# Performance work log

Measured on AMD Instinct MI355X. Metric: run time of the kernel, lower is better.

Reference implementation:

```python
import jax, jax.numpy as jnp
import numpy as np
from jax import lax

EPS_LN = 1e-5
EPS_NORM = 1e-12
NUM_HEADS = 8
KV_HEADS = 2
REP = NUM_HEADS // KV_HEADS


def _layernorm_c(x, w, b):
    # WithBias LayerNorm over channel dim; x: [b,c,h,w]
    mu = x.mean(axis=1, keepdims=True)
    var = ((x - mu) ** 2).mean(axis=1, keepdims=True)
    return (x - mu) / jnp.sqrt(var + EPS_LN) * w[None, :, None, None] + b[None, :, None, None]


def _conv1x1(x, w):
    # x: [b,c,h,w], w: [o,c]
    return jnp.einsum('bchw,oc->bohw', x, w)


def _dwconv3x3(x, w):
    # depthwise 3x3, SAME padding; w: [C,1,3,3]
    C = x.shape[1]
    return lax.conv_general_dilated(
        x, w, window_strides=(1, 1), padding='SAME',
        dimension_numbers=('NCHW', 'OIHW', 'NCHW'), feature_group_count=C)


def _l2norm(x):
    # normalize over last axis (torch F.normalize semantics)
    n = jnp.sqrt(jnp.sum(x * x, axis=-1, keepdims=True))
    return x / jnp.maximum(n, EPS_NORM)


def setup_inputs() -> dict:
    key = jax.random.key(0)
    ks = jax.random.split(key, 8)
    b, dim, h, w = 4, 192, 256, 256
    kv_ch = 2 * dim // REP  # 96
    return {
        'x': jax.random.normal(ks[0], (b, dim, h, w), jnp.float32),
        'ln_w': jnp.ones((dim,), jnp.float32),
        'ln_b': jnp.zeros((dim,), jnp.float32),
        'q_w': jax.random.normal(ks[1], (dim, dim), jnp.float32) * 0.02,
        'q_dw': jax.random.normal(ks[2], (dim, 1, 3, 3), jnp.float32) * 0.1,
        'kv_w': jax.random.normal(ks[3], (kv_ch, dim), jnp.float32) * 0.02,
        'kv_dw': jax.random.normal(ks[4], (kv_ch, 1, 3, 3), jnp.float32) * 0.1,
        'proj_w': jax.random.normal(ks[5], (dim, dim), jnp.float32) * 0.02,
        'temperature': jnp.ones((NUM_HEADS, 1, 1), jnp.float32),
    }


def reference(x, ln_w, ln_b, q_w, q_dw, kv_w, kv_dw, proj_w, temperature):
    b, c, h, w = x.shape
    xn = _layernorm_c(x, ln_w, ln_b)
    q = _dwconv3x3(_conv1x1(xn, q_w), q_dw)            # [b, c, h, w]
    kv = _dwconv3x3(_conv1x1(xn, kv_w), kv_dw)         # [b, 2c/rep, h, w]
    k, v = jnp.split(kv, 2, axis=1)
    hw = h * w
    ch = c // NUM_HEADS
    q = q.reshape(b, NUM_HEADS, ch, hw)
    k = k.reshape(b, KV_HEADS, ch, hw)
    v = v.reshape(b, KV_HEADS, ch, hw)
    k = jnp.repeat(k, REP, axis=1)                     # repeat_kv
    v = jnp.repeat(v, REP, axis=1)
    q = _l2norm(q)
    k = _l2norm(k)
    attn = jnp.einsum('bhcn,bhdn->bhcd', q, k) * temperature[None]
    attn = jax.nn.softmax(attn, axis=-1)
    out = jnp.einsum('bhcd,bhdn->bhcn', attn, v)
    out = out.reshape(b, c, h, w)
    return _conv1x1(out, proj_w)
```

## Files before the change

### kernel.cpp

```cpp
#include <hip/hip_runtime.h>
#include <hip/hip_bf16.h>
#include <stdint.h>

#define HW    65536
#define NB    4
#define CIN   192
#define OYC   288
#define BSTR  200
#define EPS2  264

__device__ __forceinline__ float bflo(unsigned u){ return __uint_as_float(u << 16); }
__device__ __forceinline__ float bfhi(unsigned u){ return __uint_as_float(u & 0xffff0000u); }
__device__ __forceinline__ float bf2f(__hip_bfloat16 v){ return __bfloat162float(v); }
__device__ __forceinline__ unsigned short f2bfbits(float f){
  __hip_bfloat16 h = __float2bfloat16(f); return *(unsigned short*)&h;
}

__device__ __forceinline__ void unpack8(uint4 u, float* f) {
  f[0]=bflo(u.x); f[1]=bfhi(u.x); f[2]=bflo(u.y); f[3]=bfhi(u.y);
  f[4]=bflo(u.z); f[5]=bfhi(u.z); f[6]=bflo(u.w); f[7]=bfhi(u.w);
}

union BF8 { uint4 u; __hip_bfloat16 h[8]; };

typedef __attribute__((ext_vector_type(8))) short short8;
typedef __attribute__((ext_vector_type(4))) float floatx4;

__global__ void k_prep(const float* __restrict__ qw, const float* __restrict__ kvw,
                       const float* __restrict__ lnw, const float* __restrict__ lnb,
                       __hip_bfloat16* __restrict__ AF, float* __restrict__ bias,
                       float* __restrict__ Ssum) {
  int blk = blockIdx.x, t = threadIdx.x;
  if (blk < 32) {
    for (int i = blk * 256 + t; i < OYC * CIN; i += 32 * 256) {
      int o = i / CIN, c = i % CIN;
      float w = (o < 192) ? qw[o * 192 + c] : kvw[(o - 192) * 192 + c];
      float val = w * lnw[c];
      int ot = o >> 4, lo = o & 15;
      int ks = c >> 5, cr = c & 31, q = cr >> 3, j = cr & 7;
      int dst = (((ot * 6 + ks) * 64) + q * 16 + lo) * 8 + j;
      AF[dst] = __float2bfloat16(val);
    }
  } else {
    for (int o = t; o < OYC; o += 256) {
      float s = 0.f, s2 = 0.f;
      for (int c = 0; c < CIN; ++c) {
        float w = (o < 192) ? qw[o * 192 + c] : kvw[(o - 192) * 192 + c];
        s += w * lnb[c];
        s2 += bf2f(__float2bfloat16(w * lnw[c]));
      }
      bias[o] = s;
      Ssum[o] = s2;
    }
  }
}

__global__ __launch_bounds__(512, 2) void k_conv1r(const float* __restrict__ x,
                                                   const __hip_bfloat16* __restrict__ AF,
                                                   const float* __restrict__ bias,
                                                   const float* __restrict__ Ssum,
                                                   __hip_bfloat16* __restrict__ y) {
  __shared__ __align__(16) __hip_bfloat16 Bl[256 * BSTR];
  __shared__ float part_s[8][256];
  __shared__ float part_q[8][256];
  __shared__ float murs[256][2];
  __shared__ float biasl[OYC];
  __shared__ float Sl[OYC];

  int bid = blockIdx.x;
  int b = bid >> 8;
  int r = bid & 255;
  int tid = threadIdx.x;
  int w = tid >> 6, l = tid & 63;

  for (int i = tid; i < OYC; i += 512) { biasl[i] = bias[i]; Sl[i] = Ssum[i]; }

  {
    const float* xb = x + (size_t)(b * CIN + w * 24) * HW + r * 256 + l * 4;
    float s[4] = {0.f, 0.f, 0.f, 0.f}, q2[4] = {0.f, 0.f, 0.f, 0.f};
    unsigned pk[4][12];
#pragma unroll
    for (int c = 0; c < 24; ++c) {
      float4 v4 = *(const float4*)(xb + (size_t)c * HW);
      float vv[4] = {v4.x, v4.y, v4.z, v4.w};
#pragma unroll
      for (int i = 0; i < 4; ++i) {
        s[i] += vv[i]; q2[i] += vv[i] * vv[i];
        unsigned bits = f2bfbits(vv[i]);
        if ((c & 1) == 0) pk[i][c >> 1] = bits;
        else              pk[i][c >> 1] |= bits << 16;
      }
    }
#pragma unroll
    for (int i = 0; i < 4; ++i) {
      int px = l * 4 + i;
#pragma unroll
      for (int j = 0; j < 3; ++j) {
        uint4 u = make_uint4(pk[i][j*4], pk[i][j*4+1], pk[i][j*4+2], pk[i][j*4+3]);
        *(uint4*)&Bl[px * BSTR + w * 24 + j * 8] = u;
      }
    }
    *(float4*)&part_s[w][l * 4] = make_float4(s[0], s[1], s[2], s[3]);
    *(float4*)&part_q[w][l * 4] = make_float4(q2[0], q2[1], q2[2], q2[3]);
  }
  __syncthreads();

  int lane = tid & 63;
  int mh = w >> 2, nq = w & 3;
  int li = lane & 15, qd = lane >> 4;

  floatx4 acc[9][4];
#pragma unroll
  for (int t = 0; t < 9; ++t)
#pragma unroll
    for (int nt = 0; nt < 4; ++nt) acc[t][nt] = (floatx4){0.f, 0.f, 0.f, 0.f};

  const __hip_bfloat16* abase = AF + ((size_t)(mh * 9) * 6 * 64 + lane) * 8;
  short8 a0[9], a1[9];
#pragma unroll
  for (int t = 0; t < 9; ++t) a0[t] = *(const short8*)(abase + (size_t)(t * 6) * 512);

#pragma unroll
  for (int ks = 0; ks < 6; ++ks) {
    short8 bf[4];
#pragma unroll
    for (int nt = 0; nt < 4; ++nt) {
      int px = nq * 64 + nt * 16 + li;
      bf[nt] = *(const short8*)&Bl[px * BSTR + ks * 32 + qd * 8];
    }
    if (ks < 5) {
#pragma unroll
      for (int t = 0; t < 9; ++t) {
        short8 v = *(const short8*)(abase + (size_t)(t * 6 + ks + 1) * 512);
        if (ks & 1) a0[t] = v; else a1[t] = v;
      }
    }
#pragma unroll
    for (int t = 0; t < 9; ++t) {
      short8 af = (ks & 1) ? a1[t] : a0[t];
#pragma unroll
      for (int nt = 0; nt < 4; ++nt)
        acc[t][nt] = __builtin_amdgcn_mfma_f32_16x16x32_bf16(af, bf[nt], acc[t][nt], 0, 0, 0);
    }
  }

  if (tid < 256) {
    float s0 = 0.f, s1 = 0.f;
#pragma unroll
    for (int g = 0; g < 8; ++g) { s0 += part_s[g][tid]; s1 += part_q[g][tid]; }
    float m = s0 * (1.f / CIN);
    float var = s1 * (1.f / CIN) - m * m;
    murs[tid][0] = m;
    murs[tid][1] = rsqrtf(var + 1e-5f);
  }

  __hip_bfloat16* EP = Bl;
#pragma unroll
  for (int ph = 0; ph < 2; ++ph) {
    __syncthreads();
    if (mh == ph) {
#pragma unroll
      for (int t = 0; t < 9; ++t)
#pragma unroll
        for (int nt = 0; nt < 4; ++nt) {
          int px = nq * 64 + nt * 16 + li;
          float mu = murs[px][0], rs = murs[px][1];
#pragma unroll
          for (int rr = 0; rr < 4; ++rr) {
            int ol = t * 16 + qd * 4 + rr;
            float val = rs * (acc[t][nt][rr] - mu * Sl[ph * 144 + ol]) + biasl[ph * 144 + ol];
            EP[ol * EPS2 + px] = __float2bfloat16(val);
          }
        }
    }
    __syncthreads();
    for (int i = tid; i < 144 * 32; i += 512) {
      int row = i >> 5, seg = i & 31;
      uint4 u = *(const uint4*)&EP[row * EPS2 + seg * 8];
      *(uint4*)&y[(size_t)(b * OYC + ph * 144 + row) * HW + r * 256 + seg * 8] = u;
    }
  }
}

__global__ __launch_bounds__(256) void k_dwkv(const __hip_bfloat16* __restrict__ y,
                                              const float* __restrict__ kvdw,
                                              __hip_bfloat16* __restrict__ kbuf,
                                              __hip_bfloat16* __restrict__ vbuf,
                                              float* __restrict__ kss) {
  __shared__ __align__(16) __hip_bfloat16 stage[18 * 256];
  int bid = blockIdx.x;
  int hb = bid & 15;
  int ck = (bid >> 4) % 96;
  int b  = bid / (16 * 96);
  int tid = threadIdx.x;
  int h0 = hb * 16;

  const __hip_bfloat16* yp = y + (size_t)(b * OYC + 192 + ck) * HW;
  for (int i = tid; i < 18 * 32; i += 256) {
    int ry = i >> 5, seg = i & 31;
    int hh = h0 - 1 + ry;
    uint4 u = make_uint4(0u, 0u, 0u, 0u);
    if ((unsigned)hh < 256u) u = *(const uint4*)(yp + hh * 256 + seg * 8);
    *(uint4*)&stage[ry * 256 + seg * 8] = u;
  }
  __syncthreads();

  float w[9];
#pragma unroll
  for (int i = 0; i < 9; ++i) w[i] = kvdw[ck * 9 + i];

  int cg = tid & 31, rg = tid >> 5;
  int c0 = cg * 8;
  bool isk = (ck < 48);
  __hip_bfloat16* ob = (isk ? kbuf : vbuf) + (size_t)(b * 48 + (ck % 48)) * HW;
  float ssq = 0.f;
#pragma unroll
  for (int rr = 0; rr < 2; ++rr) {
    int orow = rg * 2 + rr;
    float o[8];
#pragma unroll
    for (int j = 0; j < 8; ++j) o[j] = 0.f;
#pragma unroll
    for (int ry = 0; ry < 3; ++ry) {
      const __hip_bfloat16* rb = &stage[(orow + ry) * 256];
      float v[8];
      unpack8(*(const uint4*)&rb[c0], v);
      float vl = (c0 > 0)       ? bf2f(rb[c0 - 1]) : 0.f;
      float vr = (c0 + 8 < 256) ? bf2f(rb[c0 + 8]) : 0.f;
      float wl = w[ry * 3], wm = w[ry * 3 + 1], wr = w[ry * 3 + 2];
      o[0] = fmaf(wl, vl, fmaf(wm, v[0], fmaf(wr, v[1], o[0])));
#pragma unroll
      for (int j = 1; j < 7; ++j)
        o[j] = fmaf(wl, v[j-1], fmaf(wm, v[j], fmaf(wr, v[j+1], o[j])));
      o[7] = fmaf(wl, v[6], fmaf(wm, v[7], fmaf(wr, vr, o[7])));
    }
    BF8 t;
#pragma unroll
    for (int j = 0; j < 8; ++j) {
      t.h[j] = __float2bfloat16(o[j]);
      if (isk) { float fv = bf2f(t.h[j]); ssq += fv * fv; }
    }
    *(uint4*)(ob + (size_t)(h0 + orow) * 256 + c0) = t.u;
  }
  if (isk) {
#pragma unroll
    for (int off = 32; off > 0; off >>= 1) ssq += __shfl_down(ssq, off);
    __shared__ float ws4[4];
    if ((tid & 63) == 0) ws4[tid >> 6] = ssq;
    __syncthreads();
    if (tid == 0) atomicAdd(&kss[b * 48 + ck], ws4[0] + ws4[1] + ws4[2] + ws4[3]);
  }
}

__global__ __launch_bounds__(256) void k_dwq(const __hip_bfloat16* __restrict__ y,
                                             const float* __restrict__ qdw,
                                             __hip_bfloat16* __restrict__ qfull,
                                             float* __restrict__ qss) {
  __shared__ __align__(16) __hip_bfloat16 stage[18 * 256];
  int bid = blockIdx.x;
  int hb = bid & 15;
  int c  = (bid >> 4) % 192;
  int b  = bid / (16 * 192);
  int tid = threadIdx.x;
  int h0 = hb * 16;

  const __hip_bfloat16* yp = y + (size_t)(b * OYC + c) * HW;
  for (int i = tid; i < 18 * 32; i += 256) {
    int ry = i >> 5, seg = i & 31;
    int hh = h0 - 1 + ry;
    uint4 u = make_uint4(0u, 0u, 0u, 0u);
    if ((unsigned)hh < 256u) u = *(const uint4*)(yp + hh * 256 + seg * 8);
    *(uint4*)&stage[ry * 256 + seg * 8] = u;
  }
  __syncthreads();

  float w[9];
#pragma unroll
  for (int i = 0; i < 9; ++i) w[i] = qdw[c * 9 + i];

  int cg = tid & 31, rg = tid >> 5;
  int c0 = cg * 8;
  __hip_bfloat16* ob = qfull + (size_t)(b * CIN + c) * HW;
  float ssq = 0.f;
#pragma unroll
  for (int rr = 0; rr < 2; ++rr) {
    int orow = rg * 2 + rr;
    float o[8];
#pragma unroll
    for (int j = 0; j < 8; ++j) o[j] = 0.f;
#pragma unroll
    for (int ry = 0; ry < 3; ++ry) {
      const __hip_bfloat16* rb = &stage[(orow + ry) * 256];
      float v[8];
      unpack8(*(const uint4*)&rb[c0], v);
      float vl = (c0 > 0)       ? bf2f(rb[c0 - 1]) : 0.f;
      float vr = (c0 + 8 < 256) ? bf2f(rb[c0 + 8]) : 0.f;
      float wl = w[ry * 3], wm = w[ry * 3 + 1], wr = w[ry * 3 + 2];
      o[0] = fmaf(wl, vl, fmaf(wm, v[0], fmaf(wr, v[1], o[0])));
#pragma unroll
      for (int j = 1; j < 7; ++j)
        o[j] = fmaf(wl, v[j-1], fmaf(wm, v[j], fmaf(wr, v[j+1], o[j])));
      o[7] = fmaf(wl, v[6], fmaf(wm, v[7], fmaf(wr, vr, o[7])));
    }
    BF8 t;
#pragma unroll
    for (int j = 0; j < 8; ++j) {
      t.h[j] = __float2bfloat16(o[j]);
      float fv = bf2f(t.h[j]); ssq += fv * fv;
    }
    *(uint4*)(ob + (size_t)(h0 + orow) * 256 + c0) = t.u;
  }
#pragma unroll
  for (int off = 32; off > 0; off >>= 1) ssq += __shfl_down(ssq, off);
  __shared__ float ws4[4];
  if ((tid & 63) == 0) ws4[tid >> 6] = ssq;
  __syncthreads();
  if (tid == 0) atomicAdd(&qss[b * 192 + c], ws4[0] + ws4[1] + ws4[2] + ws4[3]);
}

__global__ __launch_bounds__(256) void k_qk(const __hip_bfloat16* __restrict__ qfull,
                                            const __hip_bfloat16* __restrict__ kbuf,
                                            float* __restrict__ attn) {
  __shared__ float red[96 * 33];
  int bid = blockIdx.x;
  int ck  = bid & 63;
  int kvh = (bid >> 6) & 1;
  int b   = bid >> 7;
  int tid = threadIdx.x;
  int wave = tid >> 6, lane = tid & 63;
  int li = lane & 15, qd = lane >> 4;

  for (int i = tid; i < 96 * 33; i += 256) red[i] = 0.f;

  const __hip_bfloat16* qp = qfull + (size_t)(b * CIN + kvh * 96) * HW;
  const __hip_bfloat16* kp = kbuf  + (size_t)(b * 48 + kvh * 24) * HW;
  int n0 = ck * 1024 + wave * 256;

  floatx4 acc[6][2];
#pragma unroll
  for (int mt = 0; mt < 6; ++mt) {
    acc[mt][0] = (floatx4){0.f, 0.f, 0.f, 0.f};
    acc[mt][1] = (floatx4){0.f, 0.f, 0.f, 0.f};
  }

  int kr1 = 16 + li; if (kr1 > 23) kr1 = 23;
  for (int ks = 0; ks < 8; ++ks) {
    int nn = n0 + ks * 32 + qd * 8;
    short8 bk0 = *(const short8*)(kp + (size_t)li  * HW + nn);
    short8 bk1 = *(const short8*)(kp + (size_t)kr1 * HW + nn);
#pragma unroll
    for (int mt = 0; mt < 6; ++mt) {
      short8 aq = *(const short8*)(qp + (size_t)(mt * 16 + li) * HW + nn);
      acc[mt][0] = __builtin_amdgcn_mfma_f32_16x16x32_bf16(aq, bk0, acc[mt][0], 0, 0, 0);
      acc[mt][1] = __builtin_amdgcn_mfma_f32_16x16x32_bf16(aq, bk1, acc[mt][1], 0, 0, 0);
    }
  }
  __syncthreads();

#pragma unroll
  for (int mt = 0; mt < 6; ++mt) {
#pragma unroll
    for (int nt = 0; nt < 2; ++nt) {
      int n = nt * 16 + li;
      if (n < 24) {
#pragma unroll
        for (int r = 0; r < 4; ++r) {
          int m = mt * 16 + qd * 4 + r;
          atomicAdd(&red[m * 33 + n], acc[mt][nt][r]);
        }
      }
    }
  }
  __syncthreads();

  for (int i = tid; i < 96 * 24; i += 256) {
    int m = i / 24, d = i % 24;
    int head = kvh * 4 + m / 24, cp = m % 24;
    atomicAdd(&attn[(((b * 8 + head) * 24) + cp) * 24 + d], red[m * 33 + d]);
  }
}

__global__ void k_attn_final(const float* __restrict__ attn, const float* __restrict__ qss,
                             const float* __restrict__ kss, const float* __restrict__ temp,
                             const float* __restrict__ projw, float* __restrict__ Mt) {
  int b = blockIdx.x;
  int t = threadIdx.x;
  __shared__ float as_[96 * 25];
  float acc[48];
#pragma unroll
  for (int j = 0; j < 48; ++j) acc[j] = 0.f;
  for (int kvh = 0; kvh < 2; ++kvh) {
    __syncthreads();
    if (t < 96) {
      int row = kvh * 96 + t;
      int h = row / 24, cp = row % 24;
      float rq = 1.f / fmaxf(sqrtf(qss[b * 192 + row]), 1e-12f);
      float tp = temp[h];
      float lg[24]; float mx = -1e30f;
#pragma unroll
      for (int d = 0; d < 24; ++d) {
        float rk = 1.f / fmaxf(sqrtf(kss[b * 48 + kvh * 24 + d]), 1e-12f);
        float l = attn[(((b * 8 + h) * 24) + cp) * 24 + d] * rq * rk * tp;
        lg[d] = l; mx = fmaxf(mx, l);
      }
      float s = 0.f;
#pragma unroll
      for (int d = 0; d < 24; ++d) { lg[d] = __expf(lg[d] - mx); s += lg[d]; }
      float inv = 1.f / s;
#pragma unroll
      for (int d = 0; d < 24; ++d) as_[t * 25 + d] = lg[d] * inv;
    }
    __syncthreads();
    if (t < 192) {
      for (int cc = 0; cc < 96; ++cc) {
        float pw = projw[t * 192 + kvh * 96 + cc];
        const float* ar = &as_[cc * 25];
#pragma unroll
        for (int d = 0; d < 24; ++d) acc[kvh * 24 + d] = fmaf(pw, ar[d], acc[kvh * 24 + d]);
      }
    }
  }
  if (t < 192) {
#pragma unroll
    for (int j = 0; j < 48; ++j) Mt[((size_t)b * 48 + j) * 192 + t] = acc[j];
  }
}

__global__ __launch_bounds__(256) void k_out(const __hip_bfloat16* __restrict__ vbuf,
                                             const float* __restrict__ Mt,
                                             float* __restrict__ out) {
  __shared__ __align__(16) __hip_bfloat16 lv[48 * 256];
  int bid = blockIdx.x;
  int b  = bid >> 8;
  int n0 = (bid & 255) * 256;
  int tid = threadIdx.x;
  const __hip_bfloat16* vb = vbuf + (size_t)b * 48 * HW + n0;
  for (int i = tid; i < 48 * 32; i += 256) {
    int c = i >> 5, seg = i & 31;
    *(uint4*)&lv[c * 256 + seg * 8] = *(const uint4*)(vb + (size_t)c * HW + seg * 8);
  }
  __syncthreads();
  int wave = tid >> 6, ln = tid & 63;
  const float* mb = Mt + (size_t)b * 48 * 192;
  for (int ch = 0; ch < 2; ++ch) {
    int o0 = wave * 48 + ch * 24;
    float acc[24][4];
#pragma unroll
    for (int j = 0; j < 24; ++j)
#pragma unroll
      for (int e = 0; e < 4; ++e) acc[j][e] = 0.f;
    for (int c = 0; c < 48; ++c) {
      float xv[4];
      uint2 u = *(const uint2*)&lv[c * 256 + ln * 4];
      xv[0] = bflo(u.x); xv[1] = bfhi(u.x); xv[2] = bflo(u.y); xv[3] = bfhi(u.y);
      const float* mrow = mb + c * 192 + o0;
      float4 m[6];
#pragma unroll
      for (int gg = 0; gg < 6; ++gg) m[gg] = *(const float4*)(mrow + gg * 4);
      const float* mf = (const float*)&m[0];
#pragma unroll
      for (int j = 0; j < 24; ++j) {
        float mv = mf[j];
#pragma unroll
        for (int e = 0; e < 4; ++e) acc[j][e] = fmaf(mv, xv[e], acc[j][e]);
      }
    }
#pragma unroll
    for (int j = 0; j < 24; ++j) {
      float4 st = make_float4(acc[j][0], acc[j][1], acc[j][2], acc[j][3]);
      *(float4*)&out[(size_t)(b * 192 + o0 + j) * HW + n0 + ln * 4] = st;
    }
  }
}

extern "C" void kernel_launch(void* const* d_in, const int* in_sizes, int n_in,
                              void* d_out, int out_size, void* d_ws, size_t ws_size,
                              hipStream_t stream) {
  const float* x     = (const float*)d_in[0];
  const float* ln_w  = (const float*)d_in[1];
  const float* ln_b  = (const float*)d_in[2];
  const float* q_w   = (const float*)d_in[3];
  const float* q_dw  = (const float*)d_in[4];
  const float* kv_w  = (const float*)d_in[5];
  const float* kv_dw = (const float*)d_in[6];
  const float* projw = (const float*)d_in[7];
  const float* temp  = (const float*)d_in[8];
  float* out = (float*)d_out;
  float* wsf = (float*)d_ws;

  float* qss  = wsf;
  float* kss  = wsf + 768;
  float* attn = wsf + 960;
  float* Mt   = wsf + 19392;
  float* bias = wsf + 56256;
  float* Ssum = wsf + 56544;
  __hip_bfloat16* AF = (__hip_bfloat16*)(wsf + 56832);
  __hip_bfloat16* y    = (__hip_bfloat16*)(wsf + 111872);
  __hip_bfloat16* kbuf = (__hip_bfloat16*)(wsf + 37860608);
  __hip_bfloat16* vbuf = (__hip_bfloat16*)(wsf + 44152064);
  __hip_bfloat16* qfull = (__hip_bfloat16*)d_out;

  hipMemsetAsync(wsf, 0, 19392 * sizeof(float), stream);
  hipLaunchKernelGGL(k_prep, dim3(33), dim3(256), 0, stream, q_w, kv_w, ln_w, ln_b, AF, bias, Ssum);
  hipLaunchKernelGGL(k_conv1r, dim3(NB * 256), dim3(512), 0, stream, x, AF, bias, Ssum, y);
  hipLaunchKernelGGL(k_dwkv, dim3(NB * 96 * 16), dim3(256), 0, stream, y, kv_dw, kbuf, vbuf, kss);
  hipLaunchKernelGGL(k_dwq, dim3(NB * 192 * 16), dim3(256), 0, stream, y, q_dw, qfull, qss);
  hipLaunchKernelGGL(k_qk, dim3(NB * 2 * 64), dim3(256), 0, stream, qfull, kbuf, attn);
  hipLaunchKernelGGL(k_attn_final, dim3(NB), dim3(256), 0, stream, attn, qss, kss, temp, projw, Mt);
  hipLaunchKernelGGL(k_out, dim3(NB * 256), dim3(256), 0, stream, vbuf, Mt, out);
}
```

Baseline: 678.1 us.

## Split layernorm from conv1x1 GEMM and stage q/k tiles in LDS for QK

Splits the fused layernorm+1x1-conv kernel in two. A new k_ln normalizes each pixel in fp32 before bf16 rounding and writes a pixel-major bf16 buffer into spare output memory. k_mm then runs the MFMA GEMM with only a bias epilogue, which removes the Ssum correction term and should improve accuracy. The QK kernel now stages q and k chunks through shared memory with coalesced loads instead of strided per-lane global reads. The cost is an extra kernel launch and an extra write and read of the normalized activations through global memory.

```diff
diff --git a/kernel.cpp b/kernel.cpp
--- a/kernel.cpp
+++ b/kernel.cpp
@@ -28,8 +28,7 @@
 
 __global__ void k_prep(const float* __restrict__ qw, const float* __restrict__ kvw,
                        const float* __restrict__ lnw, const float* __restrict__ lnb,
-                       __hip_bfloat16* __restrict__ AF, float* __restrict__ bias,
-                       float* __restrict__ Ssum) {
+                       __hip_bfloat16* __restrict__ AF, float* __restrict__ bias) {
   int blk = blockIdx.x, t = threadIdx.x;
   if (blk < 32) {
     for (int i = blk * 256 + t; i < OYC * CIN; i += 32 * 256) {
@@ -43,69 +42,87 @@
     }
   } else {
     for (int o = t; o < OYC; o += 256) {
-      float s = 0.f, s2 = 0.f;
-      for (int c = 0; c < CIN; ++c) {
-        float w = (o < 192) ? qw[o * 192 + c] : kvw[(o - 192) * 192 + c];
-        s += w * lnb[c];
-        s2 += bf2f(__float2bfloat16(w * lnw[c]));
-      }
+      float s = 0.f;
+      for (int c = 0; c < CIN; ++c)
+        s += ((o < 192) ? qw[o * 192 + c] : kvw[(o - 192) * 192 + c]) * lnb[c];
       bias[o] = s;
-      Ssum[o] = s2;
-    }
-  }
-}
-
-__global__ __launch_bounds__(512, 2) void k_conv1r(const float* __restrict__ x,
-                                                   const __hip_bfloat16* __restrict__ AF,
-                                                   const float* __restrict__ bias,
-                                                   const float* __restrict__ Ssum,
-                                                   __hip_bfloat16* __restrict__ y) {
+    }
+  }
+}
+
+__global__ __launch_bounds__(512) void k_ln(const float* __restrict__ x,
+                                            __hip_bfloat16* __restrict__ xT) {
   __shared__ __align__(16) __hip_bfloat16 Bl[256 * BSTR];
   __shared__ float part_s[8][256];
   __shared__ float part_q[8][256];
-  __shared__ float murs[256][2];
-  __shared__ float biasl[OYC];
-  __shared__ float Sl[OYC];
-
+  __shared__ float murs_l[256][2];
   int bid = blockIdx.x;
-  int b = bid >> 8;
-  int r = bid & 255;
+  int b = bid >> 8, r = bid & 255;
   int tid = threadIdx.x;
   int w = tid >> 6, l = tid & 63;
 
-  for (int i = tid; i < OYC; i += 512) { biasl[i] = bias[i]; Sl[i] = Ssum[i]; }
-
-  {
-    const float* xb = x + (size_t)(b * CIN + w * 24) * HW + r * 256 + l * 4;
-    float s[4] = {0.f, 0.f, 0.f, 0.f}, q2[4] = {0.f, 0.f, 0.f, 0.f};
-    unsigned pk[4][12];
-#pragma unroll
-    for (int c = 0; c < 24; ++c) {
-      float4 v4 = *(const float4*)(xb + (size_t)c * HW);
-      float vv[4] = {v4.x, v4.y, v4.z, v4.w};
-#pragma unroll
-      for (int i = 0; i < 4; ++i) {
-        s[i] += vv[i]; q2[i] += vv[i] * vv[i];
-        unsigned bits = f2bfbits(vv[i]);
-        if ((c & 1) == 0) pk[i][c >> 1] = bits;
-        else              pk[i][c >> 1] |= bits << 16;
-      }
-    }
-#pragma unroll
-    for (int i = 0; i < 4; ++i) {
-      int px = l * 4 + i;
-#pragma unroll
-      for (int j = 0; j < 3; ++j) {
-        uint4 u = make_uint4(pk[i][j*4], pk[i][j*4+1], pk[i][j*4+2], pk[i][j*4+3]);
-        *(uint4*)&Bl[px * BSTR + w * 24 + j * 8] = u;
-      }
-    }
-    *(float4*)&part_s[w][l * 4] = make_float4(s[0], s[1], s[2], s[3]);
-    *(float4*)&part_q[w][l * 4] = make_float4(q2[0], q2[1], q2[2], q2[3]);
-  }
-  __syncthreads();
-
-  int lane = tid & 63;
+  const float* xb = x + (size_t)(b * CIN + w * 24) * HW + r * 256 + l * 4;
+  float xv[24][4];
+  float s[4] = {0.f,0.f,0.f,0.f}, q2[4] = {0.f,0.f,0.f,0.f};
+#pragma unroll
+  for (int c = 0; c < 24; ++c) {
+    float4 v4 = *(const float4*)(xb + (size_t)c * HW);
+    xv[c][0] = v4.x; xv[c][1] = v4.y; xv[c][2] = v4.z; xv[c][3] = v4.w;
+#pragma unroll
+    for (int i = 0; i < 4; ++i) { s[i] += xv[c][i]; q2[i] += xv[c][i] * xv[c][i]; }
+  }
+  *(float4*)&part_s[w][l * 4] = make_float4(s[0], s[1], s[2], s[3]);
+  *(float4*)&part_q[w][l * 4] = make_float4(q2[0], q2[1], q2[2], q2[3]);
+  __syncthreads();
+  if (tid < 256) {
+    float s0 = 0.f, s1 = 0.f;
+#pragma unroll
+    for (int g = 0; g < 8; ++g) { s0 += part_s[g][tid]; s1 += part_q[g][tid]; }
+    float m = s0 * (1.f / CIN);
+    float var = s1 * (1.f / CIN) - m * m;
+    murs_l[tid][0] = m;
+    murs_l[tid][1] = rsqrtf(var + 1e-5f);
+  }
+  __syncthreads();
+#pragma unroll
+  for (int i = 0; i < 4; ++i) {
+    int px = l * 4 + i;
+    float mu = murs_l[px][0], rs = murs_l[px][1];
+#pragma unroll
+    for (int c = 0; c < 24; c += 2) {
+      unsigned lo = f2bfbits((xv[c][i]     - mu) * rs);
+      unsigned hi = f2bfbits((xv[c + 1][i] - mu) * rs);
+      *(unsigned*)&Bl[px * BSTR + w * 24 + c] = lo | (hi << 16);
+    }
+  }
+  __syncthreads();
+  __hip_bfloat16* xTr = xT + (size_t)(b * 256 + r) * 49152;
+  for (int i = tid; i < 6144; i += 512) {
+    int px = i / 24, j = i % 24;
+    *(uint4*)&xTr[px * 192 + j * 8] = *(const uint4*)&Bl[px * BSTR + j * 8];
+  }
+}
+
+__global__ __launch_bounds__(512) void k_mm(const __hip_bfloat16* __restrict__ xT,
+                                            const __hip_bfloat16* __restrict__ AF,
+                                            const float* __restrict__ bias,
+                                            __hip_bfloat16* __restrict__ y) {
+  __shared__ __align__(16) __hip_bfloat16 Bl[256 * BSTR];
+  __shared__ float biasl[OYC];
+  int bid = blockIdx.x;
+  int b = bid >> 8, r = bid & 255;
+  int tid = threadIdx.x;
+
+  for (int i = tid; i < OYC; i += 512) biasl[i] = bias[i];
+
+  const __hip_bfloat16* xTr = xT + (size_t)(b * 256 + r) * 49152;
+  for (int i = tid; i < 6144; i += 512) {
+    int px = i / 24, j = i % 24;
+    *(uint4*)&Bl[px * BSTR + j * 8] = *(const uint4*)&xTr[px * 192 + j * 8];
+  }
+  __syncthreads();
+
+  int w = tid >> 6, lane = tid & 63;
   int mh = w >> 2, nq = w & 3;
   int li = lane & 15, qd = lane >> 4;
 
@@ -144,16 +161,6 @@
     }
   }
 
-  if (tid < 256) {
-    float s0 = 0.f, s1 = 0.f;
-#pragma unroll
-    for (int g = 0; g < 8; ++g) { s0 += part_s[g][tid]; s1 += part_q[g][tid]; }
-    float m = s0 * (1.f / CIN);
-    float var = s1 * (1.f / CIN) - m * m;
-    murs[tid][0] = m;
-    murs[tid][1] = rsqrtf(var + 1e-5f);
-  }
-
   __hip_bfloat16* EP = Bl;
 #pragma unroll
   for (int ph = 0; ph < 2; ++ph) {
@@ -164,12 +171,10 @@
 #pragma unroll
         for (int nt = 0; nt < 4; ++nt) {
           int px = nq * 64 + nt * 16 + li;
-          float mu = murs[px][0], rs = murs[px][1];
 #pragma unroll
           for (int rr = 0; rr < 4; ++rr) {
             int ol = t * 16 + qd * 4 + rr;
-            float val = rs * (acc[t][nt][rr] - mu * Sl[ph * 144 + ol]) + biasl[ph * 144 + ol];
-            EP[ol * EPS2 + px] = __float2bfloat16(val);
+            EP[ol * EPS2 + px] = __float2bfloat16(acc[t][nt][rr] + biasl[ph * 144 + ol]);
           }
         }
     }
@@ -321,6 +326,8 @@
 __global__ __launch_bounds__(256) void k_qk(const __hip_bfloat16* __restrict__ qfull,
                                             const __hip_bfloat16* __restrict__ kbuf,
                                             float* __restrict__ attn) {
+  __shared__ __align__(16) __hip_bfloat16 ql[96 * 264];
+  __shared__ __align__(16) __hip_bfloat16 kl[24 * 264];
   __shared__ float red[96 * 33];
   int bid = blockIdx.x;
   int ck  = bid & 63;
@@ -332,9 +339,8 @@
 
   for (int i = tid; i < 96 * 33; i += 256) red[i] = 0.f;
 
-  const __hip_bfloat16* qp = qfull + (size_t)(b * CIN + kvh * 96) * HW;
-  const __hip_bfloat16* kp = kbuf  + (size_t)(b * 48 + kvh * 24) * HW;
-  int n0 = ck * 1024 + wave * 256;
+  const __hip_bfloat16* qp = qfull + (size_t)(b * CIN + kvh * 96) * HW + ck * 1024;
+  const __hip_bfloat16* kp = kbuf  + (size_t)(b * 48 + kvh * 24) * HW + ck * 1024;
 
   floatx4 acc[6][2];
 #pragma unroll
@@ -344,18 +350,30 @@
   }
 
   int kr1 = 16 + li; if (kr1 > 23) kr1 = 23;
-  for (int ks = 0; ks < 8; ++ks) {
-    int nn = n0 + ks * 32 + qd * 8;
-    short8 bk0 = *(const short8*)(kp + (size_t)li  * HW + nn);
-    short8 bk1 = *(const short8*)(kp + (size_t)kr1 * HW + nn);
-#pragma unroll
-    for (int mt = 0; mt < 6; ++mt) {
-      short8 aq = *(const short8*)(qp + (size_t)(mt * 16 + li) * HW + nn);
-      acc[mt][0] = __builtin_amdgcn_mfma_f32_16x16x32_bf16(aq, bk0, acc[mt][0], 0, 0, 0);
-      acc[mt][1] = __builtin_amdgcn_mfma_f32_16x16x32_bf16(aq, bk1, acc[mt][1], 0, 0, 0);
-    }
-  }
-  __syncthreads();
+  for (int sc = 0; sc < 4; ++sc) {
+    __syncthreads();
+    for (int i = tid; i < 96 * 32; i += 256) {
+      int row = i >> 5, seg = i & 31;
+      *(uint4*)&ql[row * 264 + seg * 8] = *(const uint4*)(qp + (size_t)row * HW + sc * 256 + seg * 8);
+    }
+    for (int i = tid; i < 24 * 32; i += 256) {
+      int row = i >> 5, seg = i & 31;
+      *(uint4*)&kl[row * 264 + seg * 8] = *(const uint4*)(kp + (size_t)row * HW + sc * 256 + seg * 8);
+    }
+    __syncthreads();
+#pragma unroll
+    for (int ks = 0; ks < 2; ++ks) {
+      int off = wave * 64 + ks * 32 + qd * 8;
+      short8 bk0 = *(const short8*)&kl[li  * 264 + off];
+      short8 bk1 = *(const short8*)&kl[kr1 * 264 + off];
+#pragma unroll
+      for (int mt = 0; mt < 6; ++mt) {
+        short8 aq = *(const short8*)&ql[(mt * 16 + li) * 264 + off];
+        acc[mt][0] = __builtin_amdgcn_mfma_f32_16x16x32_bf16(aq, bk0, acc[mt][0], 0, 0, 0);
+        acc[mt][1] = __builtin_amdgcn_mfma_f32_16x16x32_bf16(aq, bk1, acc[mt][1], 0, 0, 0);
+      }
+    }
+  }
 
 #pragma unroll
   for (int mt = 0; mt < 6; ++mt) {
@@ -493,19 +511,20 @@
   float* attn = wsf + 960;
   float* Mt   = wsf + 19392;
   float* bias = wsf + 56256;
-  float* Ssum = wsf + 56544;
   __hip_bfloat16* AF = (__hip_bfloat16*)(wsf + 56832);
   __hip_bfloat16* y    = (__hip_bfloat16*)(wsf + 111872);
   __hip_bfloat16* kbuf = (__hip_bfloat16*)(wsf + 37860608);
   __hip_bfloat16* vbuf = (__hip_bfloat16*)(wsf + 44152064);
   __hip_bfloat16* qfull = (__hip_bfloat16*)d_out;
+  __hip_bfloat16* xT    = (__hip_bfloat16*)((char*)d_out + 100663296);
 
   hipMemsetAsync(wsf, 0, 19392 * sizeof(float), stream);
-  hipLaunchKernelGGL(k_prep, dim3(33), dim3(256), 0, stream, q_w, kv_w, ln_w, ln_b, AF, bias, Ssum);
-  hipLaunchKernelGGL(k_conv1r, dim3(NB * 256), dim3(512), 0, stream, x, AF, bias, Ssum, y);
+  hipLaunchKernelGGL(k_prep, dim3(33), dim3(256), 0, stream, q_w, kv_w, ln_w, ln_b, AF, bias);
+  hipLaunchKernelGGL(k_ln,   dim3(NB * 256), dim3(512), 0, stream, x, xT);
+  hipLaunchKernelGGL(k_mm,   dim3(NB * 256), dim3(512), 0, stream, xT, AF, bias, y);
   hipLaunchKernelGGL(k_dwkv, dim3(NB * 96 * 16), dim3(256), 0, stream, y, kv_dw, kbuf, vbuf, kss);
-  hipLaunchKernelGGL(k_dwq, dim3(NB * 192 * 16), dim3(256), 0, stream, y, q_dw, qfull, qss);
-  hipLaunchKernelGGL(k_qk, dim3(NB * 2 * 64), dim3(256), 0, stream, qfull, kbuf, attn);
+  hipLaunchKernelGGL(k_dwq,  dim3(NB * 192 * 16), dim3(256), 0, stream, y, q_dw, qfull, qss);
+  hipLaunchKernelGGL(k_qk,   dim3(NB * 2 * 64), dim3(256), 0, stream, qfull, kbuf, attn);
   hipLaunchKernelGGL(k_attn_final, dim3(NB), dim3(256), 0, stream, attn, qss, kss, temp, projw, Mt);
-  hipLaunchKernelGGL(k_out, dim3(NB * 256), dim3(256), 0, stream, vbuf, Mt, out);
-}
+  hipLaunchKernelGGL(k_out,  dim3(NB * 256), dim3(256), 0, stream, vbuf, Mt, out);
+}
```

After: 704.1 us. +3.8%, slower.

## Use MFMA with split-bf16 weights for output projection; stage QK tiles in LDS

Applied to the files above, without the earlier changes.

The output kernel drops its scalar fp32 FMA loop and uses bf16 MFMA instead. The fused attention-projection matrix is split into bf16 hi and lo parts, packed as a K=96 operand in MFMA lane order, and multiplied against a transposed V tile held in shared memory. Results are staged through LDS so that global stores are coalesced. The QK kernel now loads Q and K chunks into padded LDS before its MFMAs rather than doing strided global short8 loads, which adds more barriers and extra LDS use in exchange for better load coalescing.

```diff
diff --git a/kernel.cpp b/kernel.cpp
--- a/kernel.cpp
+++ b/kernel.cpp
@@ -321,6 +321,8 @@
 __global__ __launch_bounds__(256) void k_qk(const __hip_bfloat16* __restrict__ qfull,
                                             const __hip_bfloat16* __restrict__ kbuf,
                                             float* __restrict__ attn) {
+  __shared__ __align__(16) __hip_bfloat16 ql[96 * 264];
+  __shared__ __align__(16) __hip_bfloat16 kl[24 * 264];
   __shared__ float red[96 * 33];
   int bid = blockIdx.x;
   int ck  = bid & 63;
@@ -332,9 +334,8 @@
 
   for (int i = tid; i < 96 * 33; i += 256) red[i] = 0.f;
 
-  const __hip_bfloat16* qp = qfull + (size_t)(b * CIN + kvh * 96) * HW;
-  const __hip_bfloat16* kp = kbuf  + (size_t)(b * 48 + kvh * 24) * HW;
-  int n0 = ck * 1024 + wave * 256;
+  const __hip_bfloat16* qp = qfull + (size_t)(b * CIN + kvh * 96) * HW + ck * 1024;
+  const __hip_bfloat16* kp = kbuf  + (size_t)(b * 48 + kvh * 24) * HW + ck * 1024;
 
   floatx4 acc[6][2];
 #pragma unroll
@@ -344,18 +345,30 @@
   }
 
   int kr1 = 16 + li; if (kr1 > 23) kr1 = 23;
-  for (int ks = 0; ks < 8; ++ks) {
-    int nn = n0 + ks * 32 + qd * 8;
-    short8 bk0 = *(const short8*)(kp + (size_t)li  * HW + nn);
-    short8 bk1 = *(const short8*)(kp + (size_t)kr1 * HW + nn);
-#pragma unroll
-    for (int mt = 0; mt < 6; ++mt) {
-      short8 aq = *(const short8*)(qp + (size_t)(mt * 16 + li) * HW + nn);
-      acc[mt][0] = __builtin_amdgcn_mfma_f32_16x16x32_bf16(aq, bk0, acc[mt][0], 0, 0, 0);
-      acc[mt][1] = __builtin_amdgcn_mfma_f32_16x16x32_bf16(aq, bk1, acc[mt][1], 0, 0, 0);
-    }
-  }
-  __syncthreads();
+  for (int sc = 0; sc < 4; ++sc) {
+    __syncthreads();
+    for (int i = tid; i < 96 * 32; i += 256) {
+      int row = i >> 5, seg = i & 31;
+      *(uint4*)&ql[row * 264 + seg * 8] = *(const uint4*)(qp + (size_t)row * HW + sc * 256 + seg * 8);
+    }
+    for (int i = tid; i < 24 * 32; i += 256) {
+      int row = i >> 5, seg = i & 31;
+      *(uint4*)&kl[row * 264 + seg * 8] = *(const uint4*)(kp + (size_t)row * HW + sc * 256 + seg * 8);
+    }
+    __syncthreads();
+#pragma unroll
+    for (int ks = 0; ks < 2; ++ks) {
+      int off = wave * 64 + ks * 32 + qd * 8;
+      short8 bk0 = *(const short8*)&kl[li  * 264 + off];
+      short8 bk1 = *(const short8*)&kl[kr1 * 264 + off];
+#pragma unroll
+      for (int mt = 0; mt < 6; ++mt) {
+        short8 aq = *(const short8*)&ql[(mt * 16 + li) * 264 + off];
+        acc[mt][0] = __builtin_amdgcn_mfma_f32_16x16x32_bf16(aq, bk0, acc[mt][0], 0, 0, 0);
+        acc[mt][1] = __builtin_amdgcn_mfma_f32_16x16x32_bf16(aq, bk1, acc[mt][1], 0, 0, 0);
+      }
+    }
+  }
 
 #pragma unroll
   for (int mt = 0; mt < 6; ++mt) {
@@ -382,7 +395,7 @@
 
 __global__ void k_attn_final(const float* __restrict__ attn, const float* __restrict__ qss,
                              const float* __restrict__ kss, const float* __restrict__ temp,
-                             const float* __restrict__ projw, float* __restrict__ Mt) {
+                             const float* __restrict__ projw, __hip_bfloat16* __restrict__ AB) {
   int b = blockIdx.x;
   int t = threadIdx.x;
   __shared__ float as_[96 * 25];
@@ -421,54 +434,107 @@
     }
   }
   if (t < 192) {
-#pragma unroll
-    for (int j = 0; j < 48; ++j) Mt[((size_t)b * 48 + j) * 192 + t] = acc[j];
-  }
-}
-
-__global__ __launch_bounds__(256) void k_out(const __hip_bfloat16* __restrict__ vbuf,
-                                             const float* __restrict__ Mt,
+    __hip_bfloat16* ABb = AB + (size_t)b * 18432;
+    int mt = t >> 4, lb = t & 15;
+#pragma unroll
+    for (int g = 0; g < 12; ++g) {
+      int kk0 = g * 8;
+      int s = kk0 >> 5;
+      int lane = lb + 16 * ((kk0 & 31) >> 3);
+      BF8 u;
+#pragma unroll
+      for (int jj = 0; jj < 8; ++jj) {
+        int kk = kk0 + jj;
+        if (kk < 48) {
+          u.h[jj] = __float2bfloat16(acc[kk]);
+        } else {
+          int j = kk - 48;
+          float hv = bf2f(__float2bfloat16(acc[j]));
+          u.h[jj] = __float2bfloat16(acc[j] - hv);
+        }
+      }
+      *(uint4*)(ABb + (size_t)((mt * 3 + s) * 64 + lane) * 8) = u.u;
+    }
+  }
+}
+
+__global__ __launch_bounds__(512) void k_out(const __hip_bfloat16* __restrict__ vbuf,
+                                             const __hip_bfloat16* __restrict__ AB,
                                              float* __restrict__ out) {
-  __shared__ __align__(16) __hip_bfloat16 lv[48 * 256];
+  __shared__ __align__(16) __hip_bfloat16 vT[256 * 56];
+  __shared__ __align__(16) float EPu[48 * 260];
+  __hip_bfloat16* vl = (__hip_bfloat16*)EPu;
+
   int bid = blockIdx.x;
   int b  = bid >> 8;
   int n0 = (bid & 255) * 256;
   int tid = threadIdx.x;
+
   const __hip_bfloat16* vb = vbuf + (size_t)b * 48 * HW + n0;
-  for (int i = tid; i < 48 * 32; i += 256) {
-    int c = i >> 5, seg = i & 31;
-    *(uint4*)&lv[c * 256 + seg * 8] = *(const uint4*)(vb + (size_t)c * HW + seg * 8);
-  }
-  __syncthreads();
-  int wave = tid >> 6, ln = tid & 63;
-  const float* mb = Mt + (size_t)b * 48 * 192;
-  for (int ch = 0; ch < 2; ++ch) {
-    int o0 = wave * 48 + ch * 24;
-    float acc[24][4];
-#pragma unroll
-    for (int j = 0; j < 24; ++j)
-#pragma unroll
-      for (int e = 0; e < 4; ++e) acc[j][e] = 0.f;
-    for (int c = 0; c < 48; ++c) {
-      float xv[4];
-      uint2 u = *(const uint2*)&lv[c * 256 + ln * 4];
-      xv[0] = bflo(u.x); xv[1] = bfhi(u.x); xv[2] = bflo(u.y); xv[3] = bfhi(u.y);
-      const float* mrow = mb + c * 192 + o0;
-      float4 m[6];
-#pragma unroll
-      for (int gg = 0; gg < 6; ++gg) m[gg] = *(const float4*)(mrow + gg * 4);
-      const float* mf = (const float*)&m[0];
-#pragma unroll
-      for (int j = 0; j < 24; ++j) {
-        float mv = mf[j];
-#pragma unroll
-        for (int e = 0; e < 4; ++e) acc[j][e] = fmaf(mv, xv[e], acc[j][e]);
-      }
-    }
-#pragma unroll
-    for (int j = 0; j < 24; ++j) {
-      float4 st = make_float4(acc[j][0], acc[j][1], acc[j][2], acc[j][3]);
-      *(float4*)&out[(size_t)(b * 192 + o0 + j) * HW + n0 + ln * 4] = st;
+  for (int i = tid; i < 48 * 32; i += 512) {
+    int j = i >> 5, seg = i & 31;
+    *(uint4*)&vl[j * 264 + seg * 8] = *(const uint4*)(vb + (size_t)j * HW + seg * 8);
+  }
+  __syncthreads();
+  for (int i = tid; i < 256 * 6; i += 512) {
+    int px = i & 255, j0 = (i >> 8) * 8;
+    BF8 u;
+#pragma unroll
+    for (int e = 0; e < 8; ++e) u.h[e] = vl[(j0 + e) * 264 + px];
+    *(uint4*)&vT[px * 56 + j0] = u.u;
+  }
+  __syncthreads();
+
+  int w = tid >> 6, lane = tid & 63;
+  int li = lane & 15, qd = lane >> 4;
+  int mg = w & 3;
+  int nh = w >> 2;
+
+  const __hip_bfloat16* ABb = AB + (size_t)b * 18432;
+
+  floatx4 acc[3][8];
+#pragma unroll
+  for (int m = 0; m < 3; ++m)
+#pragma unroll
+    for (int nt = 0; nt < 8; ++nt) acc[m][nt] = (floatx4){0.f, 0.f, 0.f, 0.f};
+
+#pragma unroll
+  for (int s = 0; s < 3; ++s) {
+    short8 a[3];
+#pragma unroll
+    for (int m = 0; m < 3; ++m)
+      a[m] = *(const short8*)(ABb + (size_t)(((mg * 3 + m) * 3 + s) * 64 + lane) * 8);
+    int t0 = s * 32 + qd * 8;
+    int j0 = (t0 >= 48) ? t0 - 48 : t0;
+#pragma unroll
+    for (int nt = 0; nt < 8; ++nt) {
+      int n = nh * 128 + nt * 16 + li;
+      short8 bv = *(const short8*)&vT[n * 56 + j0];
+#pragma unroll
+      for (int m = 0; m < 3; ++m)
+        acc[m][nt] = __builtin_amdgcn_mfma_f32_16x16x32_bf16(a[m], bv, acc[m][nt], 0, 0, 0);
+    }
+  }
+
+#pragma unroll
+  for (int ph = 0; ph < 4; ++ph) {
+    __syncthreads();
+    if (mg == ph) {
+#pragma unroll
+      for (int m = 0; m < 3; ++m)
+#pragma unroll
+        for (int nt = 0; nt < 8; ++nt) {
+          int col = nh * 128 + nt * 16 + li;
+#pragma unroll
+          for (int r = 0; r < 4; ++r)
+            EPu[(m * 16 + qd * 4 + r) * 260 + col] = acc[m][nt][r];
+        }
+    }
+    __syncthreads();
+    for (int i = tid; i < 48 * 64; i += 512) {
+      int row = i >> 6, c4 = (i & 63) * 4;
+      float4 v4 = *(const float4*)&EPu[row * 260 + c4];
+      *(float4*)&out[(size_t)(b * 192 + ph * 48 + row) * HW + n0 + c4] = v4;
     }
   }
 }
@@ -491,7 +557,7 @@
   float* qss  = wsf;
   float* kss  = wsf + 768;
   float* attn = wsf + 960;
-  float* Mt   = wsf + 19392;
+  __hip_bfloat16* AB = (__hip_bfloat16*)(wsf + 19392);
   float* bias = wsf + 56256;
   float* Ssum = wsf + 56544;
   __hip_bfloat16* AF = (__hip_bfloat16*)(wsf + 56832);
@@ -504,8 +570,8 @@
   hipLaunchKernelGGL(k_prep, dim3(33), dim3(256), 0, stream, q_w, kv_w, ln_w, ln_b, AF, bias, Ssum);
   hipLaunchKernelGGL(k_conv1r, dim3(NB * 256), dim3(512), 0, stream, x, AF, bias, Ssum, y);
   hipLaunchKernelGGL(k_dwkv, dim3(NB * 96 * 16), dim3(256), 0, stream, y, kv_dw, kbuf, vbuf, kss);
-  hipLaunchKernelGGL(k_dwq, dim3(NB * 192 * 16), dim3(256), 0, stream, y, q_dw, qfull, qss);
-  hipLaunchKernelGGL(k_qk, dim3(NB * 2 * 64), dim3(256), 0, stream, qfull, kbuf, attn);
-  hipLaunchKernelGGL(k_attn_final, dim3(NB), dim3(256), 0, stream, attn, qss, kss, temp, projw, Mt);
-  hipLaunchKernelGGL(k_out, dim3(NB * 256), dim3(256), 0, stream, vbuf, Mt, out);
-}
+  hipLaunchKernelGGL(k_dwq,  dim3(NB * 192 * 16), dim3(256), 0, stream, y, q_dw, qfull, qss);
+  hipLaunchKernelGGL(k_qk,   dim3(NB * 2 * 64), dim3(256), 0, stream, qfull, kbuf, attn);
+  hipLaunchKernelGGL(k_attn_final, dim3(NB), dim3(256), 0, stream, attn, qss, kss, temp, projw, AB);
+  hipLaunchKernelGGL(k_out,  dim3(NB * 256), dim3(512), 0, stream, vbuf, AB, out);
+}
```

Result: faster. 607.6 us (-10.4%).
